# Kernel tuning notes

Hardware: AMD Instinct MI355X
Metric: run time of the kernel (lower is better)

Reference implementation:

```python
import jax, jax.numpy as jnp
import numpy as np

INF = 100000.0
B, W, T, U, S, N = 64, 16, 64, 128, 20, 8


def setup_inputs() -> dict:
    key = jax.random.key(0)
    ks = jax.random.split(key, 9)
    xavier = (2.0 / (U + U)) ** 0.5
    return {
        "slot_utt_h": jax.random.normal(ks[0], (B, W, T, U), jnp.float32),
        "slot_candidate_c": jax.random.normal(ks[1], (S, U), jnp.float32),
        "status_candidate_c": jax.random.normal(ks[2], (N, U), jnp.float32),
        "position_encoding": jax.random.normal(ks[3], (B, W, S, U), jnp.float32),
        "q_status": jax.random.normal(ks[4], (B, W, N, U), jnp.float32),
        "mask": jnp.zeros((B, W, S * N), jnp.float32),
        "weight": jax.random.normal(ks[5], (U, U), jnp.float32) * xavier,  # bilinear co-attention weight [U,U]
        "W1": jax.random.normal(ks[6], (2 * U, U), jnp.float32) * 0.05,
        "b1": jnp.zeros((U,), jnp.float32),
        "W2": jax.random.normal(ks[7], (U, U), jnp.float32) * 0.05,
        "b2": jnp.zeros((U,), jnp.float32),
        "W3": jax.random.normal(ks[8], (U, 1), jnp.float32) * 0.05,
        "b3": jnp.zeros((1,), jnp.float32),
    }


def _zero_mask(p):
    # original: -(p == 0).float() * INF, added before softmax
    return jnp.where(p == 0.0, -INF, 0.0)


def reference(slot_utt_h, slot_candidate_c, status_candidate_c, position_encoding,
              q_status, mask, weight, W1, b1, W2, b2, W3, b3):
    # ---- attention over utterance tokens ----
    # p[b,w,s,t] = <slot_candidate_c[s], slot_utt_h[b,w,t]>
    p = jnp.einsum('su,bwtu->bwst', slot_candidate_c, slot_utt_h)
    p = jax.nn.softmax(p + _zero_mask(p), axis=-1)
    q_slot = jnp.einsum('bwst,bwtu->bwsu', p, slot_utt_h) + position_encoding  # [B,W,S,U]

    # ---- bilinear co-attention: [B,W*S,U] @ weight @ [B,U,W*N] -> [B,W,S,W,N] ----
    co = jnp.einsum('bwsu,uv,bxnv->bwsxn', q_slot, weight, q_status)
    p2 = jax.nn.softmax(co + _zero_mask(co), axis=3)  # softmax over the second window axis x

    # weighted sum of statuses over window axis x
    q_status_slot = jnp.einsum('bwsxn,bxnu->bwsnu', p2, q_status)  # [B,W,S,N,U]

    q_slot_exp = jnp.broadcast_to(q_slot[:, :, :, None, :], (B, W, S, N, U))
    features = jnp.concatenate([q_slot_exp, q_status_slot], axis=-1)  # [B,W,S,N,2U]

    # ---- MLP (dropout in eval mode = identity) ----
    h = jax.nn.relu(features @ W1 + b1)
    h = jax.nn.relu(h @ W2 + b2)
    logits = h @ W3 + b3  # [B,W,S,N,1]

    logits = logits.reshape(B, W, S * N)
    slot_pred_logits = jnp.max(logits + mask, axis=1)  # masked max-pool over window
    slot_pred_labels = (slot_pred_logits > 0.0).astype(jnp.float32)
    return (slot_pred_labels, S * N, slot_pred_logits)
```

## Files before the change

### kernel.cpp

```cpp
#include <hip/hip_runtime.h>
#include <math.h>

#define INF_ 100000.0f
constexpr int B_ = 64, W_ = 16, T_ = 64, U_ = 128, S_ = 20, N_ = 8;

typedef unsigned short ushort_t;
typedef __attribute__((ext_vector_type(8))) short bf16x8;
typedef __attribute__((ext_vector_type(4))) float floatx4;

static __device__ __forceinline__ unsigned short f2bf(float x) {
    unsigned int u = __float_as_uint(x);
    return (unsigned short)((u + 0x7fff + ((u >> 16) & 1)) >> 16);
}

__global__ __launch_bounds__(256) void k0_cast(
    const float* __restrict__ q_status, const float* __restrict__ weight,
    const float* __restrict__ W1, const float* __restrict__ W2,
    ushort_t* __restrict__ qstat_bf, ushort_t* __restrict__ wcomb,
    ushort_t* __restrict__ w1botT, ushort_t* __restrict__ w2T)
{
    int idx = blockIdx.x * 256 + threadIdx.x;
    if (idx < 1048576) { qstat_bf[idx] = f2bf(q_status[idx]); return; }
    idx -= 1048576;
    if (idx < 32768) {
        int j = idx >> 7, k = idx & 127;
        float v = (j < 128) ? weight[k * 128 + j] : W1[k * 128 + (j - 128)];
        wcomb[idx] = f2bf(v); return;
    }
    idx -= 32768;
    if (idx < 16384) {
        int j = idx >> 7, k = idx & 127;
        w1botT[idx] = f2bf(W1[(128 + k) * 128 + j]); return;
    }
    idx -= 16384;
    if (idx < 16384) {
        int j = idx >> 7, k = idx & 127;
        w2T[idx] = f2bf(W2[k * 128 + j]); return;
    }
}

__global__ __launch_bounds__(256) void k1_attn(
    const float* __restrict__ h,
    const float* __restrict__ c,
    const float* __restrict__ pos,
    ushort_t* __restrict__ q_slot_bf)
{
    __shared__ __align__(16) ushort_t sh_h[64 * 136];
    __shared__ __align__(16) ushort_t sh_hT[128 * 72];
    __shared__ __align__(16) ushort_t sh_c[32 * 136];
    __shared__ __align__(16) float    sh_sc[32 * 68];
    __shared__ __align__(16) ushort_t sh_P[32 * 72];

    const int bw = blockIdx.x, tid = threadIdx.x;
    const float* hb = h + (size_t)bw * 8192;
    for (int i = tid; i < 8192; i += 256) {
        int t = i >> 7, u = i & 127;
        ushort_t v = f2bf(hb[i]);
        sh_h[t * 136 + u] = v;
        sh_hT[u * 72 + t] = v;
    }
    for (int i = tid; i < 4096; i += 256) {
        int s = i >> 7;
        sh_c[s * 136 + (i & 127)] = (s < 20) ? f2bf(c[i]) : (ushort_t)0;
    }
    for (int i = tid; i < 32 * 72; i += 256) sh_P[i] = 0;
    __syncthreads();

    const int wave = tid >> 6, lane = tid & 63, m16 = lane & 15, q = lane >> 4;

#pragma unroll
    for (int ci = 0; ci < 2; ++ci) {
        int cmb = wave * 2 + ci;
        int mt = cmb >> 2, jt = cmb & 3;
        floatx4 acc = {0.f, 0.f, 0.f, 0.f};
#pragma unroll
        for (int kt = 0; kt < 4; ++kt) {
            bf16x8 a = *(const bf16x8*)&sh_c[(mt * 16 + m16) * 136 + kt * 32 + q * 8];
            bf16x8 b = *(const bf16x8*)&sh_h[(jt * 16 + m16) * 136 + kt * 32 + q * 8];
            acc = __builtin_amdgcn_mfma_f32_16x16x32_bf16(a, b, acc, 0, 0, 0);
        }
#pragma unroll
        for (int reg = 0; reg < 4; ++reg)
            sh_sc[(mt * 16 + q * 4 + reg) * 68 + jt * 16 + m16] = acc[reg];
    }
    __syncthreads();

    for (int s = wave; s < 20; s += 4) {
        float v = sh_sc[s * 68 + lane];
        if (v == 0.0f) v = -INF_;
        float m = v;
        for (int d = 32; d; d >>= 1) m = fmaxf(m, __shfl_xor(m, d));
        float e = expf(v - m);
        float sum = e;
        for (int d = 32; d; d >>= 1) sum += __shfl_xor(sum, d);
        sh_P[s * 72 + lane] = f2bf(e / sum);
    }
    __syncthreads();

    const size_t obase = (size_t)bw * 2560;
#pragma unroll
    for (int ci = 0; ci < 4; ++ci) {
        int cmb = wave * 4 + ci;
        int mt = cmb >> 3, jt = cmb & 7;
        floatx4 acc = {0.f, 0.f, 0.f, 0.f};
#pragma unroll
        for (int kt = 0; kt < 2; ++kt) {
            bf16x8 a = *(const bf16x8*)&sh_P[(mt * 16 + m16) * 72 + kt * 32 + q * 8];
            bf16x8 b = *(const bf16x8*)&sh_hT[(jt * 16 + m16) * 72 + kt * 32 + q * 8];
            acc = __builtin_amdgcn_mfma_f32_16x16x32_bf16(a, b, acc, 0, 0, 0);
        }
        int u = jt * 16 + m16;
#pragma unroll
        for (int reg = 0; reg < 4; ++reg) {
            int row = mt * 16 + q * 4 + reg;
            if (row < 20)
                q_slot_bf[obase + row * 128 + u] =
                    f2bf(acc[reg] + pos[obase + row * 128 + u]);
        }
    }
}

__global__ __launch_bounds__(512, 2) void k2a(
    const ushort_t* __restrict__ qs_bf,
    const ushort_t* __restrict__ wcomb,
    const float* __restrict__ b1,
    ushort_t* __restrict__ qw_bf,
    float* __restrict__ A)
{
    __shared__ __align__(16) ushort_t sh_w[256 * 136];
    const int tid = threadIdx.x;
    for (int i = tid * 4; i < 32768; i += 2048) {
        int j = i >> 7, k = i & 127;
        *(ushort4*)&sh_w[j * 136 + k] = *(const ushort4*)&wcomb[i];
    }
    __syncthreads();

    const int wave = tid >> 6, lane = tid & 63, m16 = lane & 15, q = lane >> 4;
    const size_t row = (size_t)blockIdx.x * 128 + wave * 16 + m16;

    floatx4 acc[16];
#pragma unroll
    for (int jt = 0; jt < 16; ++jt) acc[jt] = (floatx4){0.f, 0.f, 0.f, 0.f};

#pragma unroll
    for (int kt = 0; kt < 4; ++kt) {
        bf16x8 a = *(const bf16x8*)&qs_bf[row * 128 + kt * 32 + q * 8];
#pragma unroll
        for (int jt = 0; jt < 16; ++jt) {
            bf16x8 b = *(const bf16x8*)&sh_w[(jt * 16 + m16) * 136 + kt * 32 + q * 8];
            acc[jt] = __builtin_amdgcn_mfma_f32_16x16x32_bf16(a, b, acc[jt], 0, 0, 0);
        }
    }

    const size_t orow0 = (size_t)blockIdx.x * 128 + wave * 16 + q * 4;
#pragma unroll
    for (int jt = 0; jt < 16; ++jt) {
        int col = jt * 16 + m16;
        if (col < 128) {
#pragma unroll
            for (int reg = 0; reg < 4; ++reg)
                qw_bf[(orow0 + reg) * 128 + col] = f2bf(acc[jt][reg]);
        } else {
            float bv = b1[col - 128];
#pragma unroll
            for (int reg = 0; reg < 4; ++reg)
                A[(orow0 + reg) * 128 + (col - 128)] = acc[jt][reg] + bv;
        }
    }
}

__global__ __launch_bounds__(256) void k2b(
    const ushort_t* __restrict__ qstat_bf,
    const ushort_t* __restrict__ w1botT,
    ushort_t* __restrict__ qs1T_bf)
{
    __shared__ __align__(16) ushort_t sh_w[128 * 136];
    const int tid = threadIdx.x;
    for (int i = tid * 4; i < 16384; i += 1024) {
        int j = i >> 7, k = i & 127;
        *(ushort4*)&sh_w[j * 136 + k] = *(const ushort4*)&w1botT[i];
    }
    __syncthreads();

    const int wave = tid >> 6, lane = tid & 63, m16 = lane & 15, q = lane >> 4;
    const size_t row = (size_t)blockIdx.x * 64 + wave * 16 + m16;

    floatx4 acc[8];
#pragma unroll
    for (int jt = 0; jt < 8; ++jt) acc[jt] = (floatx4){0.f, 0.f, 0.f, 0.f};
#pragma unroll
    for (int kt = 0; kt < 4; ++kt) {
        bf16x8 a = *(const bf16x8*)&qstat_bf[row * 128 + kt * 32 + q * 8];
#pragma unroll
        for (int jt = 0; jt < 8; ++jt) {
            bf16x8 b = *(const bf16x8*)&sh_w[(jt * 16 + m16) * 136 + kt * 32 + q * 8];
            acc[jt] = __builtin_amdgcn_mfma_f32_16x16x32_bf16(a, b, acc[jt], 0, 0, 0);
        }
    }
    const size_t orow0 = (size_t)blockIdx.x * 64 + wave * 16 + q * 4;
#pragma unroll
    for (int jt = 0; jt < 8; ++jt) {
        int col = jt * 16 + m16;
#pragma unroll
        for (int reg = 0; reg < 4; ++reg) {
            size_t grow = orow0 + reg;
            qs1T_bf[(grow >> 7) * 16384 + (size_t)col * 128 + (grow & 127)]
                = f2bf(acc[jt][reg]);
        }
    }
}

__global__ __launch_bounds__(256) void k3_co(
    const ushort_t* __restrict__ qw_bf,
    const ushort_t* __restrict__ qstat_bf,
    float* __restrict__ co)
{
    __shared__ __align__(16) ushort_t sh_y[128 * 136];
    const int tid = threadIdx.x, rt = blockIdx.x, b = blockIdx.y;
    for (int i = tid * 4; i < 16384; i += 1024) {
        int j = i >> 7, k = i & 127;
        *(ushort4*)&sh_y[j * 136 + k] = *(const ushort4*)&qstat_bf[(size_t)b * 16384 + i];
    }
    __syncthreads();

    const int wave = tid >> 6, lane = tid & 63, m16 = lane & 15, q = lane >> 4;
    const size_t rbase = (size_t)b * 320 + rt * 64 + wave * 16;

    floatx4 acc[8];
#pragma unroll
    for (int jt = 0; jt < 8; ++jt) acc[jt] = (floatx4){0.f, 0.f, 0.f, 0.f};
#pragma unroll
    for (int kt = 0; kt < 4; ++kt) {
        bf16x8 a = *(const bf16x8*)&qw_bf[(rbase + m16) * 128 + kt * 32 + q * 8];
#pragma unroll
        for (int jt = 0; jt < 8; ++jt) {
            bf16x8 b2_ = *(const bf16x8*)&sh_y[(jt * 16 + m16) * 136 + kt * 32 + q * 8];
            acc[jt] = __builtin_amdgcn_mfma_f32_16x16x32_bf16(a, b2_, acc[jt], 0, 0, 0);
        }
    }
#pragma unroll
    for (int jt = 0; jt < 8; ++jt)
#pragma unroll
        for (int reg = 0; reg < 4; ++reg)
            co[(rbase + q * 4 + reg) * 128 + jt * 16 + m16] = acc[jt][reg];
}

__global__ __launch_bounds__(640, 5) void k4_fused(
    const float* __restrict__ co,
    const ushort_t* __restrict__ qs1T_bf,
    const float* __restrict__ A,
    const ushort_t* __restrict__ w2T,
    const float* __restrict__ b2,
    const float* __restrict__ W3,
    const float* __restrict__ b3,
    float* __restrict__ lg)
{
    __shared__ __align__(16) ushort_t sh_w2t[128 * 136];
    __shared__ __align__(16) ushort_t sh_u[160 * 136];

    const int bw = blockIdx.x, b = bw >> 4, tid = threadIdx.x;

    for (int i = tid * 4; i < 16384; i += 2560) {
        int r = i >> 7, k = i & 127;
        *(ushort4*)&sh_w2t[r * 136 + k] = *(const ushort4*)&w2T[i];
        *(ushort4*)&sh_u[r * 136 + k] = *(const ushort4*)&qs1T_bf[(size_t)b * 16384 + i];
    }

    if (tid < 160) {
        int s = tid >> 3, n = tid & 7;
        const float* crow = co + ((size_t)bw * 20 + s) * 128;
        float v[16];
        float m = -INFINITY;
#pragma unroll
        for (int x = 0; x < 16; ++x) {
            float t = crow[x * 8 + n];
            if (t == 0.0f) t = -INF_;
            v[x] = t;
            m = fmaxf(m, t);
        }
        float sum = 0.f;
#pragma unroll
        for (int x = 0; x < 16; ++x) { v[x] = expf(v[x] - m); sum += v[x]; }
        float r = 1.0f / sum;
#pragma unroll
        for (int x = 0; x < 16; ++x)
            sh_u[17408 + s * 132 + x * 8 + n] = f2bf(v[x] * r);
    }
    __syncthreads();

    const int wave = tid >> 6, lane = tid & 63, m16 = lane & 15, q = lane >> 4;
    const int n = m16 & 7;
    const int sIdx = wave * 2 + (m16 >> 3);
    const int rowS = wave * 16 + m16;

    floatx4 gacc[8];
#pragma unroll
    for (int mt = 0; mt < 8; ++mt) gacc[mt] = (floatx4){0.f, 0.f, 0.f, 0.f};

#pragma unroll
    for (int kt = 0; kt < 4; ++kt) {
        short pv = (short)sh_u[17408 + sIdx * 132 + kt * 32 + q * 8 + n];
        bf16x8 pf = {0, 0, 0, 0, 0, 0, 0, 0};
        pf[0] = (n == 0) ? pv : (short)0;
        pf[1] = (n == 1) ? pv : (short)0;
        pf[2] = (n == 2) ? pv : (short)0;
        pf[3] = (n == 3) ? pv : (short)0;
        pf[4] = (n == 4) ? pv : (short)0;
        pf[5] = (n == 5) ? pv : (short)0;
        pf[6] = (n == 6) ? pv : (short)0;
        pf[7] = (n == 7) ? pv : (short)0;
#pragma unroll
        for (int mt = 0; mt < 8; ++mt) {
            bf16x8 af = *(const bf16x8*)&sh_u[(mt * 16 + m16) * 136 + kt * 32 + q * 8];
            gacc[mt] = __builtin_amdgcn_mfma_f32_16x16x32_bf16(af, pf, gacc[mt], 0, 0, 0);
        }
    }
    __syncthreads();

    {
        const float* Ab = A + ((size_t)bw * 20 + sIdx) * 128;
#pragma unroll
        for (int mt = 0; mt < 8; ++mt) {
            int u0 = mt * 16 + q * 4;
            float4 av = *(const float4*)&Ab[u0];
            ushort4 o;
            o.x = f2bf(fmaxf(gacc[mt][0] + av.x, 0.f));
            o.y = f2bf(fmaxf(gacc[mt][1] + av.y, 0.f));
            o.z = f2bf(fmaxf(gacc[mt][2] + av.z, 0.f));
            o.w = f2bf(fmaxf(gacc[mt][3] + av.w, 0.f));
            *(ushort4*)&sh_u[rowS * 136 + u0] = o;
        }
    }
    __syncthreads();

    floatx4 acc[8];
#pragma unroll
    for (int jt = 0; jt < 8; ++jt) acc[jt] = (floatx4){0.f, 0.f, 0.f, 0.f};

#pragma unroll
    for (int kt = 0; kt < 4; ++kt) {
        const int k0 = kt * 32 + q * 8;
        bf16x8 af = *(const bf16x8*)&sh_u[rowS * 136 + k0];
#pragma unroll
        for (int jt = 0; jt < 8; ++jt) {
            bf16x8 bfr = *(const bf16x8*)&sh_w2t[(jt * 16 + m16) * 136 + k0];
            acc[jt] = __builtin_amdgcn_mfma_f32_16x16x32_bf16(af, bfr, acc[jt], 0, 0, 0);
        }
    }

    float b2v[8], w3v[8];
#pragma unroll
    for (int jt = 0; jt < 8; ++jt) {
        b2v[jt] = b2[jt * 16 + m16];
        w3v[jt] = W3[jt * 16 + m16];
    }
    const float b3v = b3[0];

#pragma unroll
    for (int reg = 0; reg < 4; ++reg) {
        float p = 0.f;
#pragma unroll
        for (int jt = 0; jt < 8; ++jt)
            p += fmaxf(acc[jt][reg] + b2v[jt], 0.f) * w3v[jt];
        p += __shfl_xor(p, 1);
        p += __shfl_xor(p, 2);
        p += __shfl_xor(p, 4);
        p += __shfl_xor(p, 8);
        if (m16 == 0)
            lg[(size_t)bw * 160 + wave * 16 + q * 4 + reg] = p + b3v;
    }
}

__global__ __launch_bounds__(256) void k5_final(
    const float* __restrict__ lg,
    const float* __restrict__ mask,
    float* __restrict__ out)
{
    int idx = blockIdx.x * 256 + threadIdx.x;
    const int SN = S_ * N_;
    if (idx < B_ * SN) {
        int b = idx / SN, sn = idx % SN;
        float m = -INFINITY;
        for (int w = 0; w < W_; ++w) {
            float v = lg[((size_t)b * W_ + w) * SN + sn] + mask[((size_t)b * W_ + w) * SN + sn];
            m = fmaxf(m, v);
        }
        out[idx] = (m > 0.f) ? 1.f : 0.f;
        out[B_ * SN + 1 + idx] = m;
    }
    if (idx == 0) out[B_ * SN] = (float)SN;
}

extern "C" void kernel_launch(void* const* d_in, const int* in_sizes, int n_in,
                              void* d_out, int out_size, void* d_ws, size_t ws_size,
                              hipStream_t stream) {
    const float* slot_utt_h = (const float*)d_in[0];
    const float* slot_candidate_c = (const float*)d_in[1];
    const float* position_encoding = (const float*)d_in[3];
    const float* q_status = (const float*)d_in[4];
    const float* mask = (const float*)d_in[5];
    const float* weight = (const float*)d_in[6];
    const float* W1 = (const float*)d_in[7];
    const float* b1 = (const float*)d_in[8];
    const float* W2 = (const float*)d_in[9];
    const float* b2 = (const float*)d_in[10];
    const float* W3 = (const float*)d_in[11];
    const float* b3 = (const float*)d_in[12];
    float* out = (float*)d_out;

    float* f = (float*)d_ws;
    ushort_t* q_slot_bf = (ushort_t*)(f + 0);
    ushort_t* qw_bf     = (ushort_t*)(f + 1310720);
    float*    A         = f + 2621440;
    ushort_t* qs1T_bf   = (ushort_t*)(f + 5242880);
    float*    co        = f + 5767168;
    float*    lg        = f + 8388608;
    ushort_t* qstat_bf  = (ushort_t*)(f + 8552448);
    ushort_t* wcomb     = (ushort_t*)(f + 9076736);
    ushort_t* w1botT    = (ushort_t*)(f + 9093120);
    ushort_t* w2T       = (ushort_t*)(f + 9101312);

    k0_cast<<<4352, 256, 0, stream>>>(q_status, weight, W1, W2,
                                      qstat_bf, wcomb, w1botT, w2T);
    k1_attn<<<1024, 256, 0, stream>>>(slot_utt_h, slot_candidate_c,
                                      position_encoding, q_slot_bf);
    k2b<<<128, 256, 0, stream>>>(qstat_bf, w1botT, qs1T_bf);
    k2a<<<160, 512, 0, stream>>>(q_slot_bf, wcomb, b1, qw_bf, A);
    k3_co<<<dim3(5, 64), 256, 0, stream>>>(qw_bf, qstat_bf, co);
    k4_fused<<<1024, 640, 0, stream>>>(co, qs1T_bf, A, w2T, b2, W3, b3, lg);
    k5_final<<<(B_ * S_ * N_ + 255) / 256, 256, 0, stream>>>(lg, mask, out);
}
```

Before: 199.2 us.

## Merge k2a/k2b launches, store co in bf16, read small weights from global

Several independent changes ship together. The slot-candidate bf16 cast moves into k0_cast, so k1 reads c_bf straight from global memory instead of staging it in shared memory. k2a and k2b merge into a single launch with split block roles, which saves one kernel launch. The co-attention scores are now written as bf16 to halve that traffic, and k4's softmax is spread over all 640 threads using shuffle reductions, while W2 is read directly from global memory instead of through LDS. Storing co in bf16 loses precision in the softmax input, and the global-memory B-fragment reads in k4 could be slower than LDS reads.

```diff
diff --git a/kernel.cpp b/kernel.cpp
--- a/kernel.cpp
+++ b/kernel.cpp
@@ -12,12 +12,17 @@
     unsigned int u = __float_as_uint(x);
     return (unsigned short)((u + 0x7fff + ((u >> 16) & 1)) >> 16);
 }
+static __device__ __forceinline__ float bf2f(unsigned short s) {
+    return __uint_as_float(((unsigned int)s) << 16);
+}
 
 __global__ __launch_bounds__(256) void k0_cast(
     const float* __restrict__ q_status, const float* __restrict__ weight,
     const float* __restrict__ W1, const float* __restrict__ W2,
+    const float* __restrict__ c,
     ushort_t* __restrict__ qstat_bf, ushort_t* __restrict__ wcomb,
-    ushort_t* __restrict__ w1botT, ushort_t* __restrict__ w2T)
+    ushort_t* __restrict__ w1botT, ushort_t* __restrict__ w2T,
+    ushort_t* __restrict__ c_bf)
 {
     int idx = blockIdx.x * 256 + threadIdx.x;
     if (idx < 1048576) { qstat_bf[idx] = f2bf(q_status[idx]); return; }
@@ -37,17 +42,22 @@
         int j = idx >> 7, k = idx & 127;
         w2T[idx] = f2bf(W2[k * 128 + j]); return;
     }
+    idx -= 16384;
+    if (idx < 4096) {
+        int s = idx >> 7;
+        c_bf[idx] = (s < 20) ? f2bf(c[idx]) : (ushort_t)0;
+        return;
+    }
 }
 
 __global__ __launch_bounds__(256) void k1_attn(
     const float* __restrict__ h,
-    const float* __restrict__ c,
+    const ushort_t* __restrict__ c_bf,
     const float* __restrict__ pos,
     ushort_t* __restrict__ q_slot_bf)
 {
     __shared__ __align__(16) ushort_t sh_h[64 * 136];
     __shared__ __align__(16) ushort_t sh_hT[128 * 72];
-    __shared__ __align__(16) ushort_t sh_c[32 * 136];
     __shared__ __align__(16) float    sh_sc[32 * 68];
     __shared__ __align__(16) ushort_t sh_P[32 * 72];
 
@@ -59,10 +69,6 @@
         sh_h[t * 136 + u] = v;
         sh_hT[u * 72 + t] = v;
     }
-    for (int i = tid; i < 4096; i += 256) {
-        int s = i >> 7;
-        sh_c[s * 136 + (i & 127)] = (s < 20) ? f2bf(c[i]) : (ushort_t)0;
-    }
     for (int i = tid; i < 32 * 72; i += 256) sh_P[i] = 0;
     __syncthreads();
 
@@ -75,7 +81,7 @@
         floatx4 acc = {0.f, 0.f, 0.f, 0.f};
 #pragma unroll
         for (int kt = 0; kt < 4; ++kt) {
-            bf16x8 a = *(const bf16x8*)&sh_c[(mt * 16 + m16) * 136 + kt * 32 + q * 8];
+            bf16x8 a = *(const bf16x8*)&c_bf[(mt * 16 + m16) * 128 + kt * 32 + q * 8];
             bf16x8 b = *(const bf16x8*)&sh_h[(jt * 16 + m16) * 136 + kt * 32 + q * 8];
             acc = __builtin_amdgcn_mfma_f32_16x16x32_bf16(a, b, acc, 0, 0, 0);
         }
@@ -120,92 +126,86 @@
     }
 }
 
-__global__ __launch_bounds__(512, 2) void k2a(
+__global__ __launch_bounds__(512, 2) void k2ab(
     const ushort_t* __restrict__ qs_bf,
     const ushort_t* __restrict__ wcomb,
     const float* __restrict__ b1,
+    const ushort_t* __restrict__ qstat_bf,
+    const ushort_t* __restrict__ w1botT,
     ushort_t* __restrict__ qw_bf,
-    float* __restrict__ A)
+    float* __restrict__ A,
+    ushort_t* __restrict__ qs1T_bf)
 {
     __shared__ __align__(16) ushort_t sh_w[256 * 136];
     const int tid = threadIdx.x;
-    for (int i = tid * 4; i < 32768; i += 2048) {
-        int j = i >> 7, k = i & 127;
-        *(ushort4*)&sh_w[j * 136 + k] = *(const ushort4*)&wcomb[i];
-    }
-    __syncthreads();
-
     const int wave = tid >> 6, lane = tid & 63, m16 = lane & 15, q = lane >> 4;
-    const size_t row = (size_t)blockIdx.x * 128 + wave * 16 + m16;
-
-    floatx4 acc[16];
-#pragma unroll
-    for (int jt = 0; jt < 16; ++jt) acc[jt] = (floatx4){0.f, 0.f, 0.f, 0.f};
-
-#pragma unroll
-    for (int kt = 0; kt < 4; ++kt) {
-        bf16x8 a = *(const bf16x8*)&qs_bf[row * 128 + kt * 32 + q * 8];
+
+    if (blockIdx.x < 160) {
+        for (int i = tid * 4; i < 32768; i += 2048) {
+            int j = i >> 7, k = i & 127;
+            *(ushort4*)&sh_w[j * 136 + k] = *(const ushort4*)&wcomb[i];
+        }
+        __syncthreads();
+
+        const size_t row = (size_t)blockIdx.x * 128 + wave * 16 + m16;
+        floatx4 acc[16];
+#pragma unroll
+        for (int jt = 0; jt < 16; ++jt) acc[jt] = (floatx4){0.f, 0.f, 0.f, 0.f};
+#pragma unroll
+        for (int kt = 0; kt < 4; ++kt) {
+            bf16x8 a = *(const bf16x8*)&qs_bf[row * 128 + kt * 32 + q * 8];
+#pragma unroll
+            for (int jt = 0; jt < 16; ++jt) {
+                bf16x8 b = *(const bf16x8*)&sh_w[(jt * 16 + m16) * 136 + kt * 32 + q * 8];
+                acc[jt] = __builtin_amdgcn_mfma_f32_16x16x32_bf16(a, b, acc[jt], 0, 0, 0);
+            }
+        }
+        const size_t orow0 = (size_t)blockIdx.x * 128 + wave * 16 + q * 4;
 #pragma unroll
         for (int jt = 0; jt < 16; ++jt) {
-            bf16x8 b = *(const bf16x8*)&sh_w[(jt * 16 + m16) * 136 + kt * 32 + q * 8];
-            acc[jt] = __builtin_amdgcn_mfma_f32_16x16x32_bf16(a, b, acc[jt], 0, 0, 0);
-        }
-    }
-
-    const size_t orow0 = (size_t)blockIdx.x * 128 + wave * 16 + q * 4;
-#pragma unroll
-    for (int jt = 0; jt < 16; ++jt) {
-        int col = jt * 16 + m16;
-        if (col < 128) {
-#pragma unroll
-            for (int reg = 0; reg < 4; ++reg)
-                qw_bf[(orow0 + reg) * 128 + col] = f2bf(acc[jt][reg]);
-        } else {
-            float bv = b1[col - 128];
-#pragma unroll
-            for (int reg = 0; reg < 4; ++reg)
-                A[(orow0 + reg) * 128 + (col - 128)] = acc[jt][reg] + bv;
-        }
-    }
-}
-
-__global__ __launch_bounds__(256) void k2b(
-    const ushort_t* __restrict__ qstat_bf,
-    const ushort_t* __restrict__ w1botT,
-    ushort_t* __restrict__ qs1T_bf)
-{
-    __shared__ __align__(16) ushort_t sh_w[128 * 136];
-    const int tid = threadIdx.x;
-    for (int i = tid * 4; i < 16384; i += 1024) {
-        int j = i >> 7, k = i & 127;
-        *(ushort4*)&sh_w[j * 136 + k] = *(const ushort4*)&w1botT[i];
-    }
-    __syncthreads();
-
-    const int wave = tid >> 6, lane = tid & 63, m16 = lane & 15, q = lane >> 4;
-    const size_t row = (size_t)blockIdx.x * 64 + wave * 16 + m16;
-
-    floatx4 acc[8];
-#pragma unroll
-    for (int jt = 0; jt < 8; ++jt) acc[jt] = (floatx4){0.f, 0.f, 0.f, 0.f};
-#pragma unroll
-    for (int kt = 0; kt < 4; ++kt) {
-        bf16x8 a = *(const bf16x8*)&qstat_bf[row * 128 + kt * 32 + q * 8];
+            int col = jt * 16 + m16;
+            if (col < 128) {
+#pragma unroll
+                for (int reg = 0; reg < 4; ++reg)
+                    qw_bf[(orow0 + reg) * 128 + col] = f2bf(acc[jt][reg]);
+            } else {
+                float bv = b1[col - 128];
+#pragma unroll
+                for (int reg = 0; reg < 4; ++reg)
+                    A[(orow0 + reg) * 128 + (col - 128)] = acc[jt][reg] + bv;
+            }
+        }
+    } else {
+        const int blk = blockIdx.x - 160;
+        for (int i = tid * 4; i < 16384; i += 2048) {
+            int j = i >> 7, k = i & 127;
+            *(ushort4*)&sh_w[j * 136 + k] = *(const ushort4*)&w1botT[i];
+        }
+        __syncthreads();
+
+        const size_t row = (size_t)blk * 128 + wave * 16 + m16;
+        floatx4 acc[8];
+#pragma unroll
+        for (int jt = 0; jt < 8; ++jt) acc[jt] = (floatx4){0.f, 0.f, 0.f, 0.f};
+#pragma unroll
+        for (int kt = 0; kt < 4; ++kt) {
+            bf16x8 a = *(const bf16x8*)&qstat_bf[row * 128 + kt * 32 + q * 8];
+#pragma unroll
+            for (int jt = 0; jt < 8; ++jt) {
+                bf16x8 b = *(const bf16x8*)&sh_w[(jt * 16 + m16) * 136 + kt * 32 + q * 8];
+                acc[jt] = __builtin_amdgcn_mfma_f32_16x16x32_bf16(a, b, acc[jt], 0, 0, 0);
+            }
+        }
+        const size_t orow0 = (size_t)blk * 128 + wave * 16 + q * 4;
 #pragma unroll
         for (int jt = 0; jt < 8; ++jt) {
-            bf16x8 b = *(const bf16x8*)&sh_w[(jt * 16 + m16) * 136 + kt * 32 + q * 8];
-            acc[jt] = __builtin_amdgcn_mfma_f32_16x16x32_bf16(a, b, acc[jt], 0, 0, 0);
-        }
-    }
-    const size_t orow0 = (size_t)blockIdx.x * 64 + wave * 16 + q * 4;
-#pragma unroll
-    for (int jt = 0; jt < 8; ++jt) {
-        int col = jt * 16 + m16;
-#pragma unroll
-        for (int reg = 0; reg < 4; ++reg) {
-            size_t grow = orow0 + reg;
-            qs1T_bf[(grow >> 7) * 16384 + (size_t)col * 128 + (grow & 127)]
-                = f2bf(acc[jt][reg]);
+            int col = jt * 16 + m16;
+#pragma unroll
+            for (int reg = 0; reg < 4; ++reg) {
+                size_t grow = orow0 + reg;
+                qs1T_bf[(grow >> 7) * 16384 + (size_t)col * 128 + (grow & 127)]
+                    = f2bf(acc[jt][reg]);
+            }
         }
     }
 }
@@ -213,7 +213,7 @@
 __global__ __launch_bounds__(256) void k3_co(
     const ushort_t* __restrict__ qw_bf,
     const ushort_t* __restrict__ qstat_bf,
-    float* __restrict__ co)
+    ushort_t* __restrict__ co_bf)
 {
     __shared__ __align__(16) ushort_t sh_y[128 * 136];
     const int tid = threadIdx.x, rt = blockIdx.x, b = blockIdx.y;
@@ -242,11 +242,11 @@
     for (int jt = 0; jt < 8; ++jt)
 #pragma unroll
         for (int reg = 0; reg < 4; ++reg)
-            co[(rbase + q * 4 + reg) * 128 + jt * 16 + m16] = acc[jt][reg];
+            co_bf[(rbase + q * 4 + reg) * 128 + jt * 16 + m16] = f2bf(acc[jt][reg]);
 }
 
 __global__ __launch_bounds__(640, 5) void k4_fused(
-    const float* __restrict__ co,
+    const ushort_t* __restrict__ co_bf,
     const ushort_t* __restrict__ qs1T_bf,
     const float* __restrict__ A,
     const ushort_t* __restrict__ w2T,
@@ -255,36 +255,38 @@
     const float* __restrict__ b3,
     float* __restrict__ lg)
 {
-    __shared__ __align__(16) ushort_t sh_w2t[128 * 136];
     __shared__ __align__(16) ushort_t sh_u[160 * 136];
 
     const int bw = blockIdx.x, b = bw >> 4, tid = threadIdx.x;
 
-    for (int i = tid * 4; i < 16384; i += 2560) {
-        int r = i >> 7, k = i & 127;
-        *(ushort4*)&sh_w2t[r * 136 + k] = *(const ushort4*)&w2T[i];
-        *(ushort4*)&sh_u[r * 136 + k] = *(const ushort4*)&qs1T_bf[(size_t)b * 16384 + i];
-    }
-
-    if (tid < 160) {
-        int s = tid >> 3, n = tid & 7;
-        const float* crow = co + ((size_t)bw * 20 + s) * 128;
-        float v[16];
+    for (int i = tid * 4; i < 16384; i += 2560)
+        *(ushort4*)&sh_u[(i >> 7) * 136 + (i & 127)] =
+            *(const ushort4*)&qs1T_bf[(size_t)b * 16384 + i];
+
+    {
+        int sn = tid >> 2, xi = tid & 3;
+        int s = sn >> 3, n = sn & 7;
+        const ushort_t* crow = co_bf + ((size_t)bw * 20 + s) * 128;
+        float v[4];
         float m = -INFINITY;
 #pragma unroll
-        for (int x = 0; x < 16; ++x) {
-            float t = crow[x * 8 + n];
+        for (int j = 0; j < 4; ++j) {
+            float t = bf2f(crow[(xi + 4 * j) * 8 + n]);
             if (t == 0.0f) t = -INF_;
-            v[x] = t;
+            v[j] = t;
             m = fmaxf(m, t);
         }
+        m = fmaxf(m, __shfl_xor(m, 1));
+        m = fmaxf(m, __shfl_xor(m, 2));
         float sum = 0.f;
 #pragma unroll
-        for (int x = 0; x < 16; ++x) { v[x] = expf(v[x] - m); sum += v[x]; }
+        for (int j = 0; j < 4; ++j) { v[j] = expf(v[j] - m); sum += v[j]; }
+        sum += __shfl_xor(sum, 1);
+        sum += __shfl_xor(sum, 2);
         float r = 1.0f / sum;
 #pragma unroll
-        for (int x = 0; x < 16; ++x)
-            sh_u[17408 + s * 132 + x * 8 + n] = f2bf(v[x] * r);
+        for (int j = 0; j < 4; ++j)
+            sh_u[17408 + s * 132 + (xi + 4 * j) * 8 + n] = f2bf(v[j] * r);
     }
     __syncthreads();
 
@@ -343,7 +345,7 @@
         bf16x8 af = *(const bf16x8*)&sh_u[rowS * 136 + k0];
 #pragma unroll
         for (int jt = 0; jt < 8; ++jt) {
-            bf16x8 bfr = *(const bf16x8*)&sh_w2t[(jt * 16 + m16) * 136 + k0];
+            bf16x8 bfr = *(const bf16x8*)&w2T[(jt * 16 + m16) * 128 + k0];
             acc[jt] = __builtin_amdgcn_mfma_f32_16x16x32_bf16(af, bfr, acc[jt], 0, 0, 0);
         }
     }
@@ -413,20 +415,22 @@
     ushort_t* qw_bf     = (ushort_t*)(f + 1310720);
     float*    A         = f + 2621440;
     ushort_t* qs1T_bf   = (ushort_t*)(f + 5242880);
-    float*    co        = f + 5767168;
+    ushort_t* co_bf     = (ushort_t*)(f + 5767168);
     float*    lg        = f + 8388608;
     ushort_t* qstat_bf  = (ushort_t*)(f + 8552448);
     ushort_t* wcomb     = (ushort_t*)(f + 9076736);
     ushort_t* w1botT    = (ushort_t*)(f + 9093120);
     ushort_t* w2T       = (ushort_t*)(f + 9101312);
-
-    k0_cast<<<4352, 256, 0, stream>>>(q_status, weight, W1, W2,
-                                      qstat_bf, wcomb, w1botT, w2T);
-    k1_attn<<<1024, 256, 0, stream>>>(slot_utt_h, slot_candidate_c,
+    ushort_t* c_bf      = (ushort_t*)(f + 9109504);
+
+    k0_cast<<<4368, 256, 0, stream>>>(q_status, weight, W1, W2,
+                                      slot_candidate_c,
+                                      qstat_bf, wcomb, w1botT, w2T, c_bf);
+    k1_attn<<<1024, 256, 0, stream>>>(slot_utt_h, c_bf,
                                       position_encoding, q_slot_bf);
-    k2b<<<128, 256, 0, stream>>>(qstat_bf, w1botT, qs1T_bf);
-    k2a<<<160, 512, 0, stream>>>(q_slot_bf, wcomb, b1, qw_bf, A);
-    k3_co<<<dim3(5, 64), 256, 0, stream>>>(qw_bf, qstat_bf, co);
-    k4_fused<<<1024, 640, 0, stream>>>(co, qs1T_bf, A, w2T, b2, W3, b3, lg);
+    k2ab<<<224, 512, 0, stream>>>(q_slot_bf, wcomb, b1, qstat_bf, w1botT,
+                                  qw_bf, A, qs1T_bf);
+    k3_co<<<dim3(5, 64), 256, 0, stream>>>(qw_bf, qstat_bf, co_bf);
+    k4_fused<<<1024, 640, 0, stream>>>(co_bf, qs1T_bf, A, w2T, b2, W3, b3, lg);
     k5_final<<<(B_ * S_ * N_ + 255) / 256, 256, 0, stream>>>(lg, mask, out);
 }
```

Result: slower. 222.2 us (+11.6%).
